# Performance work log

Measured on AMD Instinct MI355X. Metric: run time of the kernel, lower is better.

Reference implementation:

```python
import jax, jax.numpy as jnp
import numpy as np

# ---- 4-wire quantum gate: RX(x_w + theta_w) per wire, CNOT ring, <Z_w> per wire ----
N_WIRES = 4
DIM = 2 ** N_WIRES  # 16 statevector amplitudes

def _cnot_perm_inv():
    # CNOTs (0,1),(1,2),(2,3),(3,0) applied sequentially permute computational basis states.
    # inv[j] = k such that basis state k maps to j; then psi_new = psi_old[inv].
    inv = np.zeros(DIM, dtype=np.int32)
    for k in range(DIM):
        b = [(k >> 3) & 1, (k >> 2) & 1, (k >> 1) & 1, k & 1]  # wire 0 = MSB
        b[1] ^= b[0]; b[2] ^= b[1]; b[3] ^= b[2]; b[0] ^= b[3]
        nk = (b[0] << 3) | (b[1] << 2) | (b[2] << 1) | b[3]
        inv[nk] = k
    return jnp.asarray(inv)

_PERM = _cnot_perm_inv()
# sign[k, w] = (-1)^{bit_w(k)} for PauliZ expectation on wire w
_ZSIGN = jnp.asarray(np.array([[1.0 - 2.0 * ((k >> (3 - w)) & 1) for w in range(N_WIRES)]
                               for k in range(DIM)], dtype=np.float32))  # [16, 4]

def _qgate(angles, theta):
    # angles: [B, 4]. Encoder RX(x_w) then trainable RX(theta_w) on the same wire = RX(x_w + theta_w).
    a = (angles + theta) * 0.5
    c, s = jnp.cos(a), jnp.sin(a)
    amp = jnp.stack([c + 0j, (-1j) * s], axis=-1)  # [B, 4, 2] per-wire RX|0> amplitudes
    # product state over 4 wires -> [B, 16]
    psi = jnp.einsum('bi,bj,bk,bl->bijkl', amp[:, 0], amp[:, 1], amp[:, 2], amp[:, 3]).reshape(-1, DIM)
    psi = psi[:, _PERM]  # CNOT ring (classical basis permutation)
    probs = jnp.real(psi * jnp.conj(psi))  # [B, 16]
    return probs @ _ZSIGN  # [B, 4] PauliZ expectations


def setup_inputs() -> dict:
    key = jax.random.key(0)
    T, B, D, H, Q = 256, 2048, 128, 4, 4
    ks = jax.random.split(key, 16)
    inp = {"inputs": jax.random.normal(ks[0], (T, B, D), dtype=jnp.float32)}
    bound = 1.0 / float(np.sqrt(D + H))  # torch Linear default init range
    for j, n in enumerate(["f", "i", "u", "o"]):
        inp["W" + n] = jax.random.uniform(ks[1 + j], (Q, D + H), jnp.float32, -bound, bound)
        inp["b" + n] = jax.random.uniform(ks[5 + j], (Q,), jnp.float32, -bound, bound)
        inp["th" + n] = jax.random.normal(ks[9 + j], (Q,), dtype=jnp.float32)  # trainable RX angles
    return inp


def reference(inputs, Wf, bf, Wi, bi, Wu, bu, Wo, bo, thf, thi, thu, tho):
    B = inputs.shape[1]
    H = N_WIRES  # hidden_dim == n_qubits == 4
    h0 = jnp.zeros((B, H), dtype=inputs.dtype)
    c0 = jnp.zeros((B, H), dtype=inputs.dtype)

    def step(carry, x):
        hx, cx = carry
        comb = jnp.concatenate([x, hx], axis=1)  # [B, D+H]
        f = jax.nn.sigmoid(_qgate(comb @ Wf.T + bf, thf))
        i = jax.nn.sigmoid(_qgate(comb @ Wi.T + bi, thi))
        g = jnp.tanh(_qgate(comb @ Wu.T + bu, thu))
        o = jax.nn.sigmoid(_qgate(comb @ Wo.T + bo, tho))
        cx = f * cx + i * g
        hx = o * jnp.tanh(cx)
        return (hx, cx), hx

    (hx, cx), stacked = jax.lax.scan(step, (h0, c0), inputs)
    return (stacked, hx, cx)
```

## Files before the change

kernel.cpp:

```cpp
#include <hip/hip_runtime.h>

#define TT 256
#define BB 2048
#define DIN 128
#define DWROW 132
#define INV2PI 0.15915494309189535f
#define LOG2E  1.4426950408889634f

__device__ __forceinline__ const float* rfl_ptr(const float* p) {
    unsigned long long u = (unsigned long long)p;
    unsigned lo = __builtin_amdgcn_readfirstlane((unsigned)u);
    unsigned hi = __builtin_amdgcn_readfirstlane((unsigned)(u >> 32));
    return (const float*)(((unsigned long long)hi << 32) | lo);
}

#define DPP_BCAST(dst, src, j) \
    dst = __int_as_float(__builtin_amdgcn_update_dpp( \
        0, __float_as_int(src), (j) * 0x55, 0xF, 0xF, true))

#define SWZ(dst, src, imm) \
    dst = __int_as_float(__builtin_amdgcn_ds_swizzle(__float_as_int(src), (imm)))

__device__ __forceinline__ float tanh_f(float x) {
    float e = __builtin_amdgcn_exp2f((2.0f * LOG2E) * x);
    return 1.0f - 2.0f * __builtin_amdgcn_rcpf(1.0f + e);
}

__global__ __launch_bounds__(256) void qlstm_phase1(
    const float* __restrict__ x,
    const float* __restrict__ Wf, const float* __restrict__ bf, const float* __restrict__ thf,
    const float* __restrict__ Wi, const float* __restrict__ bi, const float* __restrict__ thi,
    const float* __restrict__ Wu, const float* __restrict__ bu, const float* __restrict__ thu,
    const float* __restrict__ Wo, const float* __restrict__ bo, const float* __restrict__ tho,
    float* __restrict__ Ax)
{
    __shared__ float4 xs[64 * 32];

    const int tid = threadIdx.x;
    const size_t tile = blockIdx.x;

    const float4* xg = (const float4*)x + tile * (64 * 32);
#pragma unroll
    for (int i = 0; i < 8; ++i) {
        int f   = i * 256 + tid;
        int row = f >> 5;
        int c4  = f & 31;
        xs[row * 32 + (c4 ^ (row & 7))] = xg[f];
    }
    __syncthreads();

    const int wv   = tid >> 6;
    const int lane = tid & 63;

    const float* Wp  = (wv == 0) ? Wf  : (wv == 1) ? Wi  : (wv == 2) ? Wu  : Wo;
    const float* bp  = (wv == 0) ? bf  : (wv == 1) ? bi  : (wv == 2) ? bu  : bo;
    const float* thp = (wv == 0) ? thf : (wv == 1) ? thi : (wv == 2) ? thu : tho;
    const float* Wg  = rfl_ptr(Wp);
    const float* bg  = rfl_ptr(bp);
    const float* thg = rfl_ptr(thp);

    float acc0 = bg[0] + thg[0];
    float acc1 = bg[1] + thg[1];
    float acc2 = bg[2] + thg[2];
    float acc3 = bg[3] + thg[3];

    const float4* xrow = xs + lane * 32;
    const int sw = lane & 7;

#pragma unroll 8
    for (int c = 0; c < 32; ++c) {
        float4 xv = xrow[c ^ sw];
        const int j = 4 * c;
        acc0 = fmaf(xv.x, Wg[0 * DWROW + j + 0], acc0);
        acc0 = fmaf(xv.y, Wg[0 * DWROW + j + 1], acc0);
        acc0 = fmaf(xv.z, Wg[0 * DWROW + j + 2], acc0);
        acc0 = fmaf(xv.w, Wg[0 * DWROW + j + 3], acc0);
        acc1 = fmaf(xv.x, Wg[1 * DWROW + j + 0], acc1);
        acc1 = fmaf(xv.y, Wg[1 * DWROW + j + 1], acc1);
        acc1 = fmaf(xv.z, Wg[1 * DWROW + j + 2], acc1);
        acc1 = fmaf(xv.w, Wg[1 * DWROW + j + 3], acc1);
        acc2 = fmaf(xv.x, Wg[2 * DWROW + j + 0], acc2);
        acc2 = fmaf(xv.y, Wg[2 * DWROW + j + 1], acc2);
        acc2 = fmaf(xv.z, Wg[2 * DWROW + j + 2], acc2);
        acc2 = fmaf(xv.w, Wg[2 * DWROW + j + 3], acc2);
        acc3 = fmaf(xv.x, Wg[3 * DWROW + j + 0], acc3);
        acc3 = fmaf(xv.y, Wg[3 * DWROW + j + 1], acc3);
        acc3 = fmaf(xv.z, Wg[3 * DWROW + j + 2], acc3);
        acc3 = fmaf(xv.w, Wg[3 * DWROW + j + 3], acc3);
    }

    float4 o;
    o.x = acc0 * INV2PI; o.y = acc1 * INV2PI;
    o.z = acc2 * INV2PI; o.w = acc3 * INV2PI;
    ((float4*)Ax)[(tile * 64 + lane) * 4 + wv] = o;
}

__global__ __launch_bounds__(64) void qlstm_phase2(
    const float* __restrict__ Ax,
    const float* __restrict__ Wf, const float* __restrict__ Wi,
    const float* __restrict__ Wu, const float* __restrict__ Wo,
    float* __restrict__ out)
{
    const int gtid = blockIdx.x * 64 + threadIdx.x;
    const int w = gtid & 3;
    const int g = (gtid >> 2) & 3;
    const int b = gtid >> 4;

    const float* Wrow = (g == 0) ? Wf : (g == 1) ? Wi : (g == 2) ? Wu : Wo;
    const float wh0 = Wrow[w * DWROW + DIN + 0] * INV2PI;
    const float wh1 = Wrow[w * DWROW + DIN + 1] * INV2PI;
    const float wh2 = Wrow[w * DWROW + DIN + 2] * INV2PI;
    const float wh3 = Wrow[w * DWROW + DIN + 3] * INV2PI;

    const float kk = (g == 2) ? (2.0f * LOG2E) : (-LOG2E);
    const float Aa = (g == 2) ? 1.0f : 0.0f;
    const float Bb = (g == 2) ? -2.0f : 1.0f;

    const size_t S = (size_t)BB * 16;
    const float* ap = Ax + (size_t)b * 16 + (g * 4 + w);

    float ar[4];
#pragma unroll
    for (int d = 0; d < 4; ++d)
        ar[d] = ap[(size_t)d * S];

    float hv0 = 0.f, hv1 = 0.f, hv2 = 0.f, hv3 = 0.f;
    float cst = 0.f;
    float h   = 0.f;

    for (int t4 = 0; t4 < TT / 4; ++t4) {
#pragma unroll
        for (int k = 0; k < 4; ++k) {
            const int t = 4 * t4 + k;
            float a = ar[k];
            int tn = t + 4; if (tn > TT - 1) tn = TT - 1;
            ar[k] = ap[(size_t)tn * S];

            float m23 = fmaf(hv2, wh2, hv3 * wh3);
            float ang = fmaf(hv0, wh0, fmaf(hv1, wh1, a)) + m23;
            float z   = __builtin_amdgcn_cosf(ang);

            float q0, q1, q2, q3;
            DPP_BCAST(q0, z, 0);
            DPP_BCAST(q1, z, 1);
            DPP_BCAST(q2, z, 2);
            DPP_BCAST(q3, z, 3);
            float t23 = q2 * q3;
            float p01 = q0 * q1;
            float G = (w == 0) ? q1 * t23
                    : (w == 1) ? p01
                    : (w == 2) ? p01 * q2
                    :            p01 * t23;

            float ex  = __builtin_amdgcn_exp2f(kk * G);
            float act = fmaf(Bb, __builtin_amdgcn_rcpf(1.0f + ex), Aa);

            float fa, ia, ua, oa;
            SWZ(fa, act, 0x013);
            SWZ(ia, act, 0x093);
            SWZ(ua, act, 0x113);
            SWZ(oa, act, 0x193);

            cst = fmaf(fa, cst, ia * ua);
            float th = tanh_f(cst);
            h = oa * th;

            if (g == 0)
                out[(size_t)t * (BB * 4) + b * 4 + w] = h;

            DPP_BCAST(hv0, h, 0);
            DPP_BCAST(hv1, h, 1);
            DPP_BCAST(hv2, h, 2);
            DPP_BCAST(hv3, h, 3);
        }
    }

    if (g == 0) {
        out[(size_t)TT * BB * 4 + b * 4 + w]          = h;
        out[(size_t)TT * BB * 4 + BB * 4 + b * 4 + w] = cst;
    }
}

extern "C" void kernel_launch(void* const* d_in, const int* in_sizes, int n_in,
                              void* d_out, int out_size, void* d_ws, size_t ws_size,
                              hipStream_t stream)
{
    const float* x   = (const float*)d_in[0];
    const float* Wf  = (const float*)d_in[1];
    const float* bf  = (const float*)d_in[2];
    const float* thf = (const float*)d_in[3];
    const float* Wi  = (const float*)d_in[4];
    const float* bi  = (const float*)d_in[5];
    const float* thi = (const float*)d_in[6];
    const float* Wu  = (const float*)d_in[7];
    const float* bu  = (const float*)d_in[8];
    const float* thu = (const float*)d_in[9];
    const float* Wo  = (const float*)d_in[10];
    const float* bo  = (const float*)d_in[11];
    const float* tho = (const float*)d_in[12];
    float* Ax   = (float*)d_ws;
    float* outp = (float*)d_out;

    qlstm_phase1<<<dim3((TT * BB) / 64), dim3(256), 0, stream>>>(
        x, Wf, bf, thf, Wi, bi, thi, Wu, bu, thu, Wo, bo, tho, Ax);
    qlstm_phase2<<<dim3((BB * 16) / 64), dim3(64), 0, stream>>>(
        Ax, Wf, Wi, Wu, Wo, outp);
}
```

Before: 444.9 us.

## Fuse projection and recurrence into one producer-consumer kernel with per-timestep flags

Merges the input-projection kernel and the sequential recurrence kernel into a single launch. The first 128 blocks act as recurrence consumers, and the remaining blocks compute projection tiles and bump a per-timestep completion counter with release atomics. Consumers spin on those counters before loading each timestep's projections, so the recurrence can overlap with the projection GEMM instead of waiting for it to finish. This adds a memset, atomic polling and agent-scope loads. It also depends on the consumer blocks being scheduled first so that spinning cannot deadlock the producers.

```diff
diff --git a/kernel.cpp b/kernel.cpp
--- a/kernel.cpp
+++ b/kernel.cpp
@@ -6,6 +6,8 @@
 #define DWROW 132
 #define INV2PI 0.15915494309189535f
 #define LOG2E  1.4426950408889634f
+#define NCONS 128
+#define NTILE ((TT * BB) / 64)
 
 __device__ __forceinline__ const float* rfl_ptr(const float* p) {
     unsigned long long u = (unsigned long long)p;
@@ -21,90 +23,94 @@
 #define SWZ(dst, src, imm) \
     dst = __int_as_float(__builtin_amdgcn_ds_swizzle(__float_as_int(src), (imm)))
 
+#define LD_AGENT(p) __hip_atomic_load((p), __ATOMIC_RELAXED, __HIP_MEMORY_SCOPE_AGENT)
+
 __device__ __forceinline__ float tanh_f(float x) {
     float e = __builtin_amdgcn_exp2f((2.0f * LOG2E) * x);
     return 1.0f - 2.0f * __builtin_amdgcn_rcpf(1.0f + e);
 }
 
-__global__ __launch_bounds__(256) void qlstm_phase1(
+__global__ __launch_bounds__(256) void qlstm_fused(
     const float* __restrict__ x,
     const float* __restrict__ Wf, const float* __restrict__ bf, const float* __restrict__ thf,
     const float* __restrict__ Wi, const float* __restrict__ bi, const float* __restrict__ thi,
     const float* __restrict__ Wu, const float* __restrict__ bu, const float* __restrict__ thu,
     const float* __restrict__ Wo, const float* __restrict__ bo, const float* __restrict__ tho,
-    float* __restrict__ Ax)
+    float* __restrict__ Ax, unsigned* __restrict__ done, float* __restrict__ out)
 {
     __shared__ float4 xs[64 * 32];
-
     const int tid = threadIdx.x;
-    const size_t tile = blockIdx.x;
-
-    const float4* xg = (const float4*)x + tile * (64 * 32);
-#pragma unroll
-    for (int i = 0; i < 8; ++i) {
-        int f   = i * 256 + tid;
-        int row = f >> 5;
-        int c4  = f & 31;
-        xs[row * 32 + (c4 ^ (row & 7))] = xg[f];
+
+    if (blockIdx.x >= NCONS) {
+        const size_t tile = blockIdx.x - NCONS;
+
+        const float4* xg = (const float4*)x + tile * (64 * 32);
+#pragma unroll
+        for (int i = 0; i < 8; ++i) {
+            int f   = i * 256 + tid;
+            int row = f >> 5;
+            int c4  = f & 31;
+            xs[row * 32 + (c4 ^ (row & 7))] = xg[f];
+        }
+        __syncthreads();
+
+        const int wv   = tid >> 6;
+        const int lane = tid & 63;
+
+        const float* Wp  = (wv == 0) ? Wf  : (wv == 1) ? Wi  : (wv == 2) ? Wu  : Wo;
+        const float* bp  = (wv == 0) ? bf  : (wv == 1) ? bi  : (wv == 2) ? bu  : bo;
+        const float* thp = (wv == 0) ? thf : (wv == 1) ? thi : (wv == 2) ? thu : tho;
+        const float* Wg  = rfl_ptr(Wp);
+        const float* bg  = rfl_ptr(bp);
+        const float* thg = rfl_ptr(thp);
+
+        float acc0 = bg[0] + thg[0];
+        float acc1 = bg[1] + thg[1];
+        float acc2 = bg[2] + thg[2];
+        float acc3 = bg[3] + thg[3];
+
+        const float4* xrow = xs + lane * 32;
+        const int sw = lane & 7;
+
+#pragma unroll 8
+        for (int c = 0; c < 32; ++c) {
+            float4 xv = xrow[c ^ sw];
+            const int j = 4 * c;
+            acc0 = fmaf(xv.x, Wg[0 * DWROW + j + 0], acc0);
+            acc0 = fmaf(xv.y, Wg[0 * DWROW + j + 1], acc0);
+            acc0 = fmaf(xv.z, Wg[0 * DWROW + j + 2], acc0);
+            acc0 = fmaf(xv.w, Wg[0 * DWROW + j + 3], acc0);
+            acc1 = fmaf(xv.x, Wg[1 * DWROW + j + 0], acc1);
+            acc1 = fmaf(xv.y, Wg[1 * DWROW + j + 1], acc1);
+            acc1 = fmaf(xv.z, Wg[1 * DWROW + j + 2], acc1);
+            acc1 = fmaf(xv.w, Wg[1 * DWROW + j + 3], acc1);
+            acc2 = fmaf(xv.x, Wg[2 * DWROW + j + 0], acc2);
+            acc2 = fmaf(xv.y, Wg[2 * DWROW + j + 1], acc2);
+            acc2 = fmaf(xv.z, Wg[2 * DWROW + j + 2], acc2);
+            acc2 = fmaf(xv.w, Wg[2 * DWROW + j + 3], acc2);
+            acc3 = fmaf(xv.x, Wg[3 * DWROW + j + 0], acc3);
+            acc3 = fmaf(xv.y, Wg[3 * DWROW + j + 1], acc3);
+            acc3 = fmaf(xv.z, Wg[3 * DWROW + j + 2], acc3);
+            acc3 = fmaf(xv.w, Wg[3 * DWROW + j + 3], acc3);
+        }
+
+        float4 o;
+        o.x = acc0 * INV2PI; o.y = acc1 * INV2PI;
+        o.z = acc2 * INV2PI; o.w = acc3 * INV2PI;
+        ((float4*)Ax)[(tile * 64 + lane) * 4 + wv] = o;
+
+        __syncthreads();
+        if (tid == 0)
+            __hip_atomic_fetch_add(&done[(unsigned)(tile >> 5)], 1u,
+                                   __ATOMIC_RELEASE, __HIP_MEMORY_SCOPE_AGENT);
+        return;
     }
-    __syncthreads();
-
-    const int wv   = tid >> 6;
+
+    const int vb   = blockIdx.x * 4 + (tid >> 6);
     const int lane = tid & 63;
-
-    const float* Wp  = (wv == 0) ? Wf  : (wv == 1) ? Wi  : (wv == 2) ? Wu  : Wo;
-    const float* bp  = (wv == 0) ? bf  : (wv == 1) ? bi  : (wv == 2) ? bu  : bo;
-    const float* thp = (wv == 0) ? thf : (wv == 1) ? thi : (wv == 2) ? thu : tho;
-    const float* Wg  = rfl_ptr(Wp);
-    const float* bg  = rfl_ptr(bp);
-    const float* thg = rfl_ptr(thp);
-
-    float acc0 = bg[0] + thg[0];
-    float acc1 = bg[1] + thg[1];
-    float acc2 = bg[2] + thg[2];
-    float acc3 = bg[3] + thg[3];
-
-    const float4* xrow = xs + lane * 32;
-    const int sw = lane & 7;
-
-#pragma unroll 8
-    for (int c = 0; c < 32; ++c) {
-        float4 xv = xrow[c ^ sw];
-        const int j = 4 * c;
-        acc0 = fmaf(xv.x, Wg[0 * DWROW + j + 0], acc0);
-        acc0 = fmaf(xv.y, Wg[0 * DWROW + j + 1], acc0);
-        acc0 = fmaf(xv.z, Wg[0 * DWROW + j + 2], acc0);
-        acc0 = fmaf(xv.w, Wg[0 * DWROW + j + 3], acc0);
-        acc1 = fmaf(xv.x, Wg[1 * DWROW + j + 0], acc1);
-        acc1 = fmaf(xv.y, Wg[1 * DWROW + j + 1], acc1);
-        acc1 = fmaf(xv.z, Wg[1 * DWROW + j + 2], acc1);
-        acc1 = fmaf(xv.w, Wg[1 * DWROW + j + 3], acc1);
-        acc2 = fmaf(xv.x, Wg[2 * DWROW + j + 0], acc2);
-        acc2 = fmaf(xv.y, Wg[2 * DWROW + j + 1], acc2);
-        acc2 = fmaf(xv.z, Wg[2 * DWROW + j + 2], acc2);
-        acc2 = fmaf(xv.w, Wg[2 * DWROW + j + 3], acc2);
-        acc3 = fmaf(xv.x, Wg[3 * DWROW + j + 0], acc3);
-        acc3 = fmaf(xv.y, Wg[3 * DWROW + j + 1], acc3);
-        acc3 = fmaf(xv.z, Wg[3 * DWROW + j + 2], acc3);
-        acc3 = fmaf(xv.w, Wg[3 * DWROW + j + 3], acc3);
-    }
-
-    float4 o;
-    o.x = acc0 * INV2PI; o.y = acc1 * INV2PI;
-    o.z = acc2 * INV2PI; o.w = acc3 * INV2PI;
-    ((float4*)Ax)[(tile * 64 + lane) * 4 + wv] = o;
-}
-
-__global__ __launch_bounds__(64) void qlstm_phase2(
-    const float* __restrict__ Ax,
-    const float* __restrict__ Wf, const float* __restrict__ Wi,
-    const float* __restrict__ Wu, const float* __restrict__ Wo,
-    float* __restrict__ out)
-{
-    const int gtid = blockIdx.x * 64 + threadIdx.x;
-    const int w = gtid & 3;
-    const int g = (gtid >> 2) & 3;
-    const int b = gtid >> 4;
+    const int w = lane & 3;
+    const int g = (lane >> 2) & 3;
+    const int b = vb * 4 + (lane >> 4);
 
     const float* Wrow = (g == 0) ? Wf : (g == 1) ? Wi : (g == 2) ? Wu : Wo;
     const float wh0 = Wrow[w * DWROW + DIN + 0] * INV2PI;
@@ -117,24 +123,45 @@
     const float Bb = (g == 2) ? -2.0f : 1.0f;
 
     const size_t S = (size_t)BB * 16;
-    const float* ap = Ax + (size_t)b * 16 + (g * 4 + w);
-
+    float* ap = Ax + (size_t)b * 16 + (g * 4 + w);
+
+#pragma unroll
+    for (int i = 0; i < 4; ++i)
+        while (LD_AGENT(&done[i]) < 32u)
+            __builtin_amdgcn_s_sleep(2);
     float ar[4];
 #pragma unroll
     for (int d = 0; d < 4; ++d)
-        ar[d] = ap[(size_t)d * S];
+        ar[d] = LD_AGENT(ap + (size_t)d * S);
 
     float hv0 = 0.f, hv1 = 0.f, hv2 = 0.f, hv3 = 0.f;
     float cst = 0.f;
     float h   = 0.f;
 
     for (int t4 = 0; t4 < TT / 4; ++t4) {
+        {
+            const int base = 4 * t4 + 4;
+            const int tw0 = (base + 0 > TT - 1) ? TT - 1 : base + 0;
+            const int tw1 = (base + 1 > TT - 1) ? TT - 1 : base + 1;
+            const int tw2 = (base + 2 > TT - 1) ? TT - 1 : base + 2;
+            const int tw3 = (base + 3 > TT - 1) ? TT - 1 : base + 3;
+            unsigned d0 = LD_AGENT(&done[tw0]);
+            unsigned d1 = LD_AGENT(&done[tw1]);
+            unsigned d2 = LD_AGENT(&done[tw2]);
+            unsigned d3 = LD_AGENT(&done[tw3]);
+            if ((d0 < 32u) | (d1 < 32u) | (d2 < 32u) | (d3 < 32u)) {
+                while (LD_AGENT(&done[tw0]) < 32u) __builtin_amdgcn_s_sleep(2);
+                while (LD_AGENT(&done[tw1]) < 32u) __builtin_amdgcn_s_sleep(2);
+                while (LD_AGENT(&done[tw2]) < 32u) __builtin_amdgcn_s_sleep(2);
+                while (LD_AGENT(&done[tw3]) < 32u) __builtin_amdgcn_s_sleep(2);
+            }
+        }
 #pragma unroll
         for (int k = 0; k < 4; ++k) {
             const int t = 4 * t4 + k;
             float a = ar[k];
             int tn = t + 4; if (tn > TT - 1) tn = TT - 1;
-            ar[k] = ap[(size_t)tn * S];
+            ar[k] = LD_AGENT(ap + (size_t)tn * S);
 
             float m23 = fmaf(hv2, wh2, hv3 * wh3);
             float ang = fmaf(hv0, wh0, fmaf(hv1, wh1, a)) + m23;
@@ -198,11 +225,14 @@
     const float* Wo  = (const float*)d_in[10];
     const float* bo  = (const float*)d_in[11];
     const float* tho = (const float*)d_in[12];
-    float* Ax   = (float*)d_ws;
-    float* outp = (float*)d_out;
-
-    qlstm_phase1<<<dim3((TT * BB) / 64), dim3(256), 0, stream>>>(
-        x, Wf, bf, thf, Wi, bi, thi, Wu, bu, thu, Wo, bo, tho, Ax);
-    qlstm_phase2<<<dim3((BB * 16) / 64), dim3(64), 0, stream>>>(
-        Ax, Wf, Wi, Wu, Wo, outp);
-}
+
+    float*    Ax   = (float*)d_ws;
+    unsigned* done = (unsigned*)((char*)d_ws + (size_t)TT * BB * 16 * 4);
+    float*    outp = (float*)d_out;
+
+    hipMemsetAsync(done, 0, TT * sizeof(unsigned), stream);
+
+    qlstm_fused<<<dim3(NCONS + NTILE), dim3(256), 0, stream>>>(
+        x, Wf, bf, thf, Wi, bi, thi, Wu, bu, thu, Wo, bo, tho,
+        Ax, done, outp);
+}
```

Result: slower. 997.6 us (+124.3%).
